# Performance work log

Measured on AMD Instinct MI355X. Metric: run time of the kernel, lower is better.

## Reference

```python
import jax, jax.numpy as jnp
import numpy as np

D_MODEL = 256
NHEAD = 8
DK = D_MODEL // NHEAD
EDGE_FEAT_DIM = 7
N_NODES = 2048
N_EDGES = 65536
LN_EPS = 1e-5


def _ln(x, g, b):
    mu = jnp.mean(x, axis=-1, keepdims=True)
    var = jnp.mean(jnp.square(x - mu), axis=-1, keepdims=True)
    return (x - mu) * jax.lax.rsqrt(var + LN_EPS) * g + b


def setup_inputs() -> dict:
    key = jax.random.key(0)
    ks = jax.random.split(key, 16)
    d, h2 = D_MODEL, 2 * D_MODEL
    s = 0.02
    inp = {
        "h": jax.random.normal(ks[0], (N_NODES, d), jnp.float32),
        "edge_attr": jax.random.normal(ks[1], (N_EDGES, EDGE_FEAT_DIM), jnp.float32),
        # weights stored as (in, out): y = x @ W + b (matches torch Linear math)
        "Wq": s * jax.random.normal(ks[2], (d, d), jnp.float32),
        "bq": jnp.zeros((d,), jnp.float32),
        "Wk": s * jax.random.normal(ks[3], (d, d), jnp.float32),
        "bk": jnp.zeros((d,), jnp.float32),
        "Wv": s * jax.random.normal(ks[4], (d, d), jnp.float32),
        "bv": jnp.zeros((d,), jnp.float32),
        "Wo": s * jax.random.normal(ks[5], (d, d), jnp.float32),
        "bo": jnp.zeros((d,), jnp.float32),
        "We": s * jax.random.normal(ks[6], (EDGE_FEAT_DIM, NHEAD), jnp.float32),
        "be": jnp.zeros((NHEAD,), jnp.float32),
        "ln1_g": jnp.ones((d,), jnp.float32),
        "ln1_b": jnp.zeros((d,), jnp.float32),
        "fln_g": jnp.ones((d,), jnp.float32),
        "fln_b": jnp.zeros((d,), jnp.float32),
        "W1": s * jax.random.normal(ks[7], (d, h2), jnp.float32),
        "b1": jnp.zeros((h2,), jnp.float32),
        "W2": s * jax.random.normal(ks[8], (h2, d), jnp.float32),
        "b2": jnp.zeros((d,), jnp.float32),
        "edge_index": jax.random.randint(ks[9], (2, N_EDGES), 0, N_NODES, jnp.int64 if jax.config.jax_enable_x64 else jnp.int32),
    }
    return inp


def reference(h, edge_attr, Wq, bq, Wk, bk, Wv, bv, Wo, bo, We, be,
              ln1_g, ln1_b, fln_g, fln_b, W1, b1, W2, b2, edge_index):
    N = h.shape[0]
    res = h
    # edge bias scattered into dense (N, N, H) tensor
    eb = edge_attr @ We + be                                  # (E, H)
    attn_bias = jnp.zeros((N, N, NHEAD), h.dtype).at[edge_index[0], edge_index[1]].set(eb)
    Q = (h @ Wq + bq).reshape(N, NHEAD, DK)
    K = (h @ Wk + bk).reshape(N, NHEAD, DK)
    V = (h @ Wv + bv).reshape(N, NHEAD, DK)
    scores = jnp.einsum('nhd,mhd->nmh', Q, K) / jnp.sqrt(jnp.float32(DK)) + attn_bias
    attn = jax.nn.softmax(scores, axis=1)                     # softmax over keys m
    out = jnp.einsum('nmh,mhd->nhd', attn, V).reshape(N, D_MODEL)
    out = out @ Wo + bo
    h1 = _ln(res + out, ln1_g, ln1_b)
    ffn = jax.nn.gelu(_ln(h1, fln_g, fln_b) @ W1 + b1, approximate=False) @ W2 + b2
    return h1 + ffn
```

## Files before the change

kernel.cpp:

```cpp
#include <hip/hip_runtime.h>
#include <math.h>

#define NN 2048
#define NE 65536
#define DM 256
#define NH 8
#define DKH 32
#define CAP 128
#define TM2 128
#define SPLIT 4

typedef __attribute__((ext_vector_type(8))) short bf16x8;
typedef __attribute__((ext_vector_type(4))) float f32x4;

__device__ __forceinline__ unsigned short f2b(float f) {
    unsigned u = __float_as_uint(f);
    unsigned r = (u + 0x7FFFu + ((u >> 16) & 1u)) >> 16;
    return (unsigned short)r;
}
__device__ __forceinline__ float b2f(unsigned short s) {
    return __uint_as_float(((unsigned)s) << 16);
}

__global__ __launch_bounds__(256) void edge_eb_kernel(
    const float* __restrict__ ea, const float* __restrict__ We,
    const float* __restrict__ be, float* __restrict__ eb)
{
    int e = blockIdx.x * 256 + threadIdx.x;
    float acc[NH];
#pragma unroll
    for (int h = 0; h < NH; ++h) acc[h] = be[h];
#pragma unroll
    for (int f = 0; f < 7; ++f) {
        float x = ea[e * 7 + f];
#pragma unroll
        for (int h = 0; h < NH; ++h) acc[h] = fmaf(x, We[f * NH + h], acc[h]);
    }
#pragma unroll
    for (int h = 0; h < NH; ++h) eb[e * NH + h] = acc[h];
}

__global__ __launch_bounds__(256) void scatter_kernel(
    const int* __restrict__ ei, int* __restrict__ cnt, int* __restrict__ lst)
{
    int e = blockIdx.x * 256 + threadIdx.x;
    int s = ei[e];
    int p = atomicAdd(&cnt[s], 1);
    if (p < CAP) lst[s * CAP + p] = e;
}

__global__ __launch_bounds__(128) void rowprep_kernel(
    const int* __restrict__ ei, const int* __restrict__ cnt,
    const int* __restrict__ lst, int* __restrict__ sortedDest,
    int* __restrict__ sortedE, int* __restrict__ rowOff)
{
    __shared__ int ds[CAP], es[CAP];
    __shared__ int bc[16], off[17];
    int n = blockIdx.x, t = threadIdx.x;
    int c = cnt[n]; if (c > CAP) c = CAP;
    if (t < 16) bc[t] = 0;
    int e = -1, d = -1;
    if (t < c) { e = lst[n * CAP + t]; d = ei[NE + e]; }
    ds[t] = d; es[t] = e;
    __syncthreads();
    bool win = (t < c);
    if (win) {
        for (int j = 0; j < c; ++j)
            if (ds[j] == d && es[j] > e) { win = false; break; }
    }
    int bkt = (d >= 0) ? (d >> 7) : 0;
    int pos = -1;
    if (win) pos = atomicAdd(&bc[bkt], 1);
    __syncthreads();
    if (t == 0) {
        int s = 0;
        for (int i = 0; i < 16; ++i) { off[i] = s; s += bc[i]; }
        off[16] = s;
    }
    __syncthreads();
    if (win) {
        int p = off[bkt] + pos;
        sortedDest[n * CAP + p] = d;
        sortedE[n * CAP + p] = e;
    }
    if (t < 17) rowOff[n * 17 + t] = off[t];
}

__global__ __launch_bounds__(256) void conv_h_kernel(
    const float* __restrict__ x, unsigned short* __restrict__ y)
{
    int i = blockIdx.x * 256 + threadIdx.x;
    y[i] = f2b(x[i]);
}

__global__ __launch_bounds__(256) void convT_kernel(
    const float* __restrict__ in, unsigned short* __restrict__ out, int K, int N)
{
    int i = blockIdx.x * 256 + threadIdx.x;
    int n = i / K, k = i - n * K;
    out[i] = f2b(in[(size_t)k * N + n]);
}

__global__ __launch_bounds__(256) void convT_qkv_kernel(
    const float* __restrict__ Wq, const float* __restrict__ Wk,
    const float* __restrict__ Wv, unsigned short* __restrict__ out)
{
    int i = blockIdx.x * 256 + threadIdx.x;
    int n = i >> 8, k = i & 255;
    const float* W = (n < 256) ? Wq : (n < 512) ? Wk : Wv;
    out[i] = f2b(W[k * 256 + (n & 255)]);
}

template <int EPI>
__global__ __launch_bounds__(128) void gemm_bf16(
    const unsigned short* __restrict__ A, const unsigned short* __restrict__ Bt,
    const float* __restrict__ bias0, const float* __restrict__ bias1,
    const float* __restrict__ bias2, const float* __restrict__ resid,
    void* __restrict__ out0, void* __restrict__ out1, void* __restrict__ out2,
    int M, int N, int K)
{
    __shared__ unsigned short As[32][40];
    __shared__ unsigned short Bs[64][40];
    int tid = threadIdx.x;
    int wv = tid >> 6, l = tid & 63, l15 = l & 15, quad = l >> 4;
    int m0 = blockIdx.y * 32, n0 = blockIdx.x * 64;

    f32x4 acc[4];
#pragma unroll
    for (int i = 0; i < 4; ++i) acc[i] = (f32x4){0.f, 0.f, 0.f, 0.f};

    int ra = tid >> 2, ka = (tid & 3) * 8;
    int rb = tid >> 1, kb = (tid & 1) * 16;

    for (int k0 = 0; k0 < K; k0 += 32) {
        *(uint4*)&As[ra][ka] = *(const uint4*)(A + (size_t)(m0 + ra) * K + k0 + ka);
        *(uint4*)&Bs[rb][kb]     = *(const uint4*)(Bt + (size_t)(n0 + rb) * K + k0 + kb);
        *(uint4*)&Bs[rb][kb + 8] = *(const uint4*)(Bt + (size_t)(n0 + rb) * K + k0 + kb + 8);
        __syncthreads();
        bf16x8 a = *(const bf16x8*)&As[wv * 16 + l15][quad * 8];
#pragma unroll
        for (int nt = 0; nt < 4; ++nt) {
            bf16x8 b = *(const bf16x8*)&Bs[nt * 16 + l15][quad * 8];
            acc[nt] = __builtin_amdgcn_mfma_f32_16x16x32_bf16(a, b, acc[nt], 0, 0, 0);
        }
        __syncthreads();
    }

#pragma unroll
    for (int nt = 0; nt < 4; ++nt) {
#pragma unroll
        for (int r = 0; r < 4; ++r) {
            int row = m0 + wv * 16 + quad * 4 + r;
            int col = n0 + nt * 16 + l15;
            float v = acc[nt][r];
            if (EPI == 0) {
                v += bias0[col];
                if (resid) v += resid[(size_t)row * N + col];
                ((float*)out0)[(size_t)row * N + col] = v;
            } else if (EPI == 1) {
                v += bias0[col];
                v = 0.5f * v * (1.0f + erff(v * 0.70710678118654752f));
                ((unsigned short*)out0)[(size_t)row * N + col] = f2b(v);
            } else {
                if (col < 256) {
                    v = (v + bias0[col]) * 0.17677669529663689f;
                    ((unsigned short*)out0)[(size_t)row * 256 + col] = f2b(v);
                } else if (col < 512) {
                    v += bias1[col - 256];
                    ((unsigned short*)out1)[(size_t)row * 256 + col - 256] = f2b(v);
                } else {
                    v += bias2[col - 512];
                    ((unsigned short*)out2)[(size_t)row * 256 + col - 512] = f2b(v);
                }
            }
        }
    }
}

__global__ __launch_bounds__(256) void vtrans_kernel(
    const unsigned short* __restrict__ Vb, unsigned short* __restrict__ Vt)
{
    __shared__ unsigned short tile[64][40];
    int h = blockIdx.y, n0 = blockIdx.x * 64, t = threadIdx.x;
    int r = t >> 2, c8 = (t & 3) * 8;
    *(uint4*)&tile[r][c8] = *(const uint4*)(Vb + (size_t)(n0 + r) * DM + h * 32 + c8);
    __syncthreads();
    int d = t >> 3, nc = (t & 7) * 8;
    unsigned short o[8];
#pragma unroll
    for (int j = 0; j < 8; ++j) o[j] = tile[nc + j][d];
    *(uint4*)(Vt + ((size_t)h * 32 + d) * NN + n0 + nc) = *(uint4*)o;
}

__global__ __launch_bounds__(128) void attn_mfma(
    const unsigned short* __restrict__ Qb, const unsigned short* __restrict__ Kb,
    const unsigned short* __restrict__ Vt, const float* __restrict__ eb,
    const int* __restrict__ sortedDest, const int* __restrict__ sortedE,
    const int* __restrict__ rowOff,
    float* __restrict__ accD, float* __restrict__ lD)
{
    __shared__ unsigned short Ks[TM2][40];
    __shared__ unsigned short Vs[32][TM2 + 8];
    __shared__ unsigned short Ps[2][16][TM2 + 16];
    __shared__ float ldelta[2][16];
    int h = blockIdx.y, tid = threadIdx.x;
    int wv = tid >> 6, l = tid & 63, l15 = l & 15, quad = l >> 4;
    int n0 = blockIdx.x * 32 + wv * 16;
    int mz = blockIdx.z;

    if (l < 16) ldelta[wv][l] = 0.f;

    bf16x8 aq = *(const bf16x8*)(Qb + (size_t)(n0 + l15) * DM + h * 32 + quad * 8);

    f32x4 oacc[2];
    oacc[0] = (f32x4){0.f, 0.f, 0.f, 0.f};
    oacc[1] = (f32x4){0.f, 0.f, 0.f, 0.f};
    float lacc[4] = {0.f, 0.f, 0.f, 0.f};
    const unsigned short* Vth = Vt + (size_t)h * 32 * NN;

    int r16 = l >> 2, sub = l & 3;
    int frow = n0 + r16;

    for (int t = 0; t < NN / (TM2 * SPLIT); ++t) {
        int m0 = (mz * (NN / SPLIT)) + t * TM2;
        int ti = m0 >> 7;
        {
            const unsigned short* ks = Kb + (size_t)(m0 + tid) * DM + h * 32;
            *(uint4*)&Ks[tid][0]  = *(const uint4*)(ks);
            *(uint4*)&Ks[tid][8]  = *(const uint4*)(ks + 8);
            *(uint4*)&Ks[tid][16] = *(const uint4*)(ks + 16);
            *(uint4*)&Ks[tid][24] = *(const uint4*)(ks + 24);
            int d = tid >> 2, mc = (tid & 3) * 32;
            const unsigned short* vs = Vth + (size_t)d * NN + m0 + mc;
            *(uint4*)&Vs[d][mc]      = *(const uint4*)(vs);
            *(uint4*)&Vs[d][mc + 8]  = *(const uint4*)(vs + 8);
            *(uint4*)&Vs[d][mc + 16] = *(const uint4*)(vs + 16);
            *(uint4*)&Vs[d][mc + 24] = *(const uint4*)(vs + 24);
        }
        __syncthreads();
#pragma unroll
        for (int mt = 0; mt < TM2 / 16; ++mt) {
            bf16x8 bk = *(const bf16x8*)&Ks[mt * 16 + l15][quad * 8];
            f32x4 s = __builtin_amdgcn_mfma_f32_16x16x32_bf16(
                aq, bk, (f32x4){0.f, 0.f, 0.f, 0.f}, 0, 0, 0);
#pragma unroll
            for (int r = 0; r < 4; ++r) {
                float p = __expf(s[r]);
                lacc[r] += p;
                Ps[wv][quad * 4 + r][mt * 16 + l15] = f2b(p);
            }
        }
        __syncthreads();
        {
            int o0 = rowOff[frow * 17 + ti];
            int o1 = rowOff[frow * 17 + ti + 1];
            for (int idx = o0 + sub; idx < o1; idx += 4) {
                int d = sortedDest[frow * CAP + idx] - m0;
                int e = sortedE[frow * CAP + idx];
                float expb = __expf(eb[e * NH + h]);
                float pold = b2f(Ps[wv][r16][d]);
                Ps[wv][r16][d] = f2b(pold * expb);
                atomicAdd(&ldelta[wv][r16], pold * (expb - 1.0f));
            }
        }
        __syncthreads();
#pragma unroll
        for (int kc = 0; kc < TM2 / 32; ++kc) {
            bf16x8 ap = *(const bf16x8*)&Ps[wv][l15][kc * 32 + quad * 8];
#pragma unroll
            for (int nt = 0; nt < 2; ++nt) {
                bf16x8 bv = *(const bf16x8*)&Vs[nt * 16 + l15][kc * 32 + quad * 8];
                oacc[nt] = __builtin_amdgcn_mfma_f32_16x16x32_bf16(ap, bv, oacc[nt], 0, 0, 0);
            }
        }
        __syncthreads();
    }

#pragma unroll
    for (int off = 1; off < 16; off <<= 1) {
#pragma unroll
        for (int r = 0; r < 4; ++r) lacc[r] += __shfl_xor(lacc[r], off);
    }
    float* lDp = lD + (size_t)mz * NN * NH;
    if (l15 == 0) {
#pragma unroll
        for (int r = 0; r < 4; ++r)
            lDp[(size_t)(n0 + quad * 4 + r) * NH + h] = lacc[r] + ldelta[wv][quad * 4 + r];
    }
    float* aDp = accD + (size_t)mz * NN * DM;
#pragma unroll
    for (int nt = 0; nt < 2; ++nt)
#pragma unroll
        for (int r = 0; r < 4; ++r)
            aDp[(size_t)(n0 + quad * 4 + r) * DM + h * 32 + nt * 16 + l15] = oacc[nt][r];
}

__global__ __launch_bounds__(256) void norm_kernel(
    const float* __restrict__ accD, const float* __restrict__ lD,
    unsigned short* __restrict__ AOb)
{
    int i = blockIdx.x * 256 + threadIdx.x;
    int n = i >> 8, cdim = i & 255, h = cdim >> 5;
    float o = 0.f, lsum = 0.f;
#pragma unroll
    for (int s = 0; s < SPLIT; ++s) {
        o += accD[(size_t)s * NN * DM + i];
        lsum += lD[(size_t)s * NN * NH + (size_t)n * NH + h];
    }
    AOb[i] = f2b(o / lsum);
}

__global__ __launch_bounds__(256) void ln2_kernel(
    const float* __restrict__ T, const float* __restrict__ g1, const float* __restrict__ b1,
    const float* __restrict__ g2, const float* __restrict__ b2,
    float* __restrict__ H1, unsigned short* __restrict__ X2b)
{
    __shared__ float red[4];
    int n = blockIdx.x, t = threadIdx.x;
    float x = T[(size_t)n * DM + t];

    float s = x;
#pragma unroll
    for (int off = 32; off; off >>= 1) s += __shfl_xor(s, off);
    if ((t & 63) == 0) red[t >> 6] = s;
    __syncthreads();
    float mu = (red[0] + red[1] + red[2] + red[3]) * (1.0f / 256.0f);
    __syncthreads();

    float d = x - mu;
    float v = d * d;
#pragma unroll
    for (int off = 32; off; off >>= 1) v += __shfl_xor(v, off);
    if ((t & 63) == 0) red[t >> 6] = v;
    __syncthreads();
    float var = (red[0] + red[1] + red[2] + red[3]) * (1.0f / 256.0f);
    float y = d * rsqrtf(var + 1e-5f) * g1[t] + b1[t];
    H1[(size_t)n * DM + t] = y;
    __syncthreads();

    float s2 = y;
#pragma unroll
    for (int off = 32; off; off >>= 1) s2 += __shfl_xor(s2, off);
    if ((t & 63) == 0) red[t >> 6] = s2;
    __syncthreads();
    float mu2 = (red[0] + red[1] + red[2] + red[3]) * (1.0f / 256.0f);
    __syncthreads();

    float d2 = y - mu2;
    float v2 = d2 * d2;
#pragma unroll
    for (int off = 32; off; off >>= 1) v2 += __shfl_xor(v2, off);
    if ((t & 63) == 0) red[t >> 6] = v2;
    __syncthreads();
    float var2 = (red[0] + red[1] + red[2] + red[3]) * (1.0f / 256.0f);
    X2b[(size_t)n * DM + t] = f2b(d2 * rsqrtf(var2 + 1e-5f) * g2[t] + b2[t]);
}

extern "C" void kernel_launch(void* const* d_in, const int* in_sizes, int n_in,
                              void* d_out, int out_size, void* d_ws, size_t ws_size,
                              hipStream_t stream)
{
    const float* h    = (const float*)d_in[0];
    const float* ea   = (const float*)d_in[1];
    const float* Wq   = (const float*)d_in[2];
    const float* bq   = (const float*)d_in[3];
    const float* Wk   = (const float*)d_in[4];
    const float* bk   = (const float*)d_in[5];
    const float* Wv   = (const float*)d_in[6];
    const float* bv   = (const float*)d_in[7];
    const float* Wo   = (const float*)d_in[8];
    const float* bo   = (const float*)d_in[9];
    const float* We   = (const float*)d_in[10];
    const float* be   = (const float*)d_in[11];
    const float* ln1g = (const float*)d_in[12];
    const float* ln1b = (const float*)d_in[13];
    const float* flng = (const float*)d_in[14];
    const float* flnb = (const float*)d_in[15];
    const float* W1   = (const float*)d_in[16];
    const float* b1   = (const float*)d_in[17];
    const float* W2   = (const float*)d_in[18];
    const float* b2   = (const float*)d_in[19];
    const int*   ei   = (const int*)d_in[20];
    float* out = (float*)d_out;

    char* p = (char*)d_ws;
    float* eb   = (float*)p;           p += (size_t)NE * NH * 4;
    int*   cnt  = (int*)p;             p += (size_t)NN * 4;
    int*   lst  = (int*)p;             p += (size_t)NN * CAP * 4;
    int*   sD   = (int*)p;             p += (size_t)NN * CAP * 4;
    int*   sE   = (int*)p;             p += (size_t)NN * CAP * 4;
    int*   rOff = (int*)p;             p += (size_t)NN * 17 * 4;
    unsigned short* hb    = (unsigned short*)p; p += (size_t)NN * DM * 2;
    unsigned short* Wqkvt = (unsigned short*)p; p += (size_t)768 * 256 * 2;
    unsigned short* Wot   = (unsigned short*)p; p += (size_t)256 * 256 * 2;
    unsigned short* W1t   = (unsigned short*)p; p += (size_t)512 * 256 * 2;
    unsigned short* W2t   = (unsigned short*)p; p += (size_t)256 * 512 * 2;
    unsigned short* Qb    = (unsigned short*)p; p += (size_t)NN * DM * 2;
    unsigned short* Kb    = (unsigned short*)p; p += (size_t)NN * DM * 2;
    unsigned short* Vb    = (unsigned short*)p; p += (size_t)NN * DM * 2;
    unsigned short* Vt    = (unsigned short*)p; p += (size_t)NN * DM * 2;
    float* accD = (float*)p;           p += (size_t)SPLIT * NN * DM * 4;
    float* lD   = (float*)p;           p += (size_t)SPLIT * NN * NH * 4;
    unsigned short* AOb   = (unsigned short*)p; p += (size_t)NN * DM * 2;
    float* T    = (float*)p;           p += (size_t)NN * DM * 4;
    float* H1   = (float*)p;           p += (size_t)NN * DM * 4;
    unsigned short* X2b   = (unsigned short*)p; p += (size_t)NN * DM * 2;
    unsigned short* F1b   = (unsigned short*)p; p += (size_t)NN * 512 * 2;

    hipMemsetAsync(cnt, 0, (size_t)NN * 4, stream);
    edge_eb_kernel<<<NE / 256, 256, 0, stream>>>(ea, We, be, eb);
    scatter_kernel<<<NE / 256, 256, 0, stream>>>(ei, cnt, lst);
    rowprep_kernel<<<NN, 128, 0, stream>>>(ei, cnt, lst, sD, sE, rOff);

    conv_h_kernel<<<NN * DM / 256, 256, 0, stream>>>(h, hb);
    convT_qkv_kernel<<<768 * 256 / 256, 256, 0, stream>>>(Wq, Wk, Wv, Wqkvt);
    convT_kernel<<<256 * 256 / 256, 256, 0, stream>>>(Wo, Wot, 256, 256);
    convT_kernel<<<512 * 256 / 256, 256, 0, stream>>>(W1, W1t, 256, 512);
    convT_kernel<<<512 * 256 / 256, 256, 0, stream>>>(W2, W2t, 512, 256);

    gemm_bf16<2><<<dim3(768 / 64, NN / 32), 128, 0, stream>>>(
        hb, Wqkvt, bq, bk, bv, nullptr, Qb, Kb, Vb, NN, 768, 256);
    vtrans_kernel<<<dim3(NN / 64, NH), 256, 0, stream>>>(Vb, Vt);

    attn_mfma<<<dim3(NN / 32, NH, SPLIT), 128, 0, stream>>>(
        Qb, Kb, Vt, eb, sD, sE, rOff, accD, lD);
    norm_kernel<<<NN * DM / 256, 256, 0, stream>>>(accD, lD, AOb);

    gemm_bf16<0><<<dim3(256 / 64, NN / 32), 128, 0, stream>>>(
        AOb, Wot, bo, nullptr, nullptr, h, T, nullptr, nullptr, NN, 256, 256);
    ln2_kernel<<<NN, 256, 0, stream>>>(T, ln1g, ln1b, flng, flnb, H1, X2b);

    gemm_bf16<1><<<dim3(512 / 64, NN / 32), 128, 0, stream>>>(
        X2b, W1t, b1, nullptr, nullptr, nullptr, F1b, nullptr, nullptr, NN, 512, 256);
    gemm_bf16<0><<<dim3(256 / 64, NN / 32), 128, 0, stream>>>(
        F1b, W2t, b2, nullptr, nullptr, H1, out, nullptr, nullptr, NN, 256, 512);
}
```

Measured before the change: 204.1 us.

## Fuse prep kernels and enlarge GEMM and attention blocks to four waves

Merges edge-bias computation with edge scatter, and folds the input and weight bf16 conversion and transpose kernels into a single launch. The bf16 GEMM gets a template row-tile size, and the QKV and W1 GEMMs use 64-row tiles with 256 threads. The attention kernel now processes 64 query rows per block with four waves, sharing each K/V tile load across more rows. The aim is less launch overhead and fewer redundant K/V and B loads, at the cost of fewer blocks and possibly lower occupancy.

```diff
diff --git a/kernel.cpp b/kernel.cpp
--- a/kernel.cpp
+++ b/kernel.cpp
@@ -22,9 +22,10 @@
     return __uint_as_float(((unsigned)s) << 16);
 }
 
-__global__ __launch_bounds__(256) void edge_eb_kernel(
+__global__ __launch_bounds__(256) void edge_prep_kernel(
     const float* __restrict__ ea, const float* __restrict__ We,
-    const float* __restrict__ be, float* __restrict__ eb)
+    const float* __restrict__ be, const int* __restrict__ ei,
+    float* __restrict__ eb, int* __restrict__ cnt, int* __restrict__ lst)
 {
     int e = blockIdx.x * 256 + threadIdx.x;
     float acc[NH];
@@ -38,12 +39,6 @@
     }
 #pragma unroll
     for (int h = 0; h < NH; ++h) eb[e * NH + h] = acc[h];
-}
-
-__global__ __launch_bounds__(256) void scatter_kernel(
-    const int* __restrict__ ei, int* __restrict__ cnt, int* __restrict__ lst)
-{
-    int e = blockIdx.x * 256 + threadIdx.x;
     int s = ei[e];
     int p = atomicAdd(&cnt[s], 1);
     if (p < CAP) lst[s * CAP + p] = e;
@@ -86,56 +81,67 @@
     if (t < 17) rowOff[n * 17 + t] = off[t];
 }
 
-__global__ __launch_bounds__(256) void conv_h_kernel(
-    const float* __restrict__ x, unsigned short* __restrict__ y)
+__global__ __launch_bounds__(256) void prep_kernel(
+    const float* __restrict__ h, const float* __restrict__ Wq,
+    const float* __restrict__ Wk, const float* __restrict__ Wv,
+    const float* __restrict__ Wo, const float* __restrict__ W1,
+    const float* __restrict__ W2,
+    unsigned short* __restrict__ hb, unsigned short* __restrict__ Wqkvt,
+    unsigned short* __restrict__ Wot, unsigned short* __restrict__ W1t,
+    unsigned short* __restrict__ W2t)
 {
     int i = blockIdx.x * 256 + threadIdx.x;
-    y[i] = f2b(x[i]);
-}
-
-__global__ __launch_bounds__(256) void convT_kernel(
-    const float* __restrict__ in, unsigned short* __restrict__ out, int K, int N)
-{
-    int i = blockIdx.x * 256 + threadIdx.x;
-    int n = i / K, k = i - n * K;
-    out[i] = f2b(in[(size_t)k * N + n]);
-}
-
-__global__ __launch_bounds__(256) void convT_qkv_kernel(
-    const float* __restrict__ Wq, const float* __restrict__ Wk,
-    const float* __restrict__ Wv, unsigned short* __restrict__ out)
-{
-    int i = blockIdx.x * 256 + threadIdx.x;
-    int n = i >> 8, k = i & 255;
-    const float* W = (n < 256) ? Wq : (n < 512) ? Wk : Wv;
-    out[i] = f2b(W[k * 256 + (n & 255)]);
-}
-
-template <int EPI>
-__global__ __launch_bounds__(128) void gemm_bf16(
+    if (i < 524288) {
+        hb[i] = f2b(h[i]);
+    } else if (i < 720896) {
+        int j = i - 524288;
+        int n = j >> 8, k = j & 255;
+        const float* W = (n < 256) ? Wq : (n < 512) ? Wk : Wv;
+        Wqkvt[j] = f2b(W[k * 256 + (n & 255)]);
+    } else if (i < 786432) {
+        int j = i - 720896;
+        int n = j >> 8, k = j & 255;
+        Wot[j] = f2b(Wo[k * 256 + n]);
+    } else if (i < 917504) {
+        int j = i - 786432;
+        int n = j >> 8, k = j & 255;
+        W1t[j] = f2b(W1[(size_t)k * 512 + n]);
+    } else {
+        int j = i - 917504;
+        int n = j >> 9, k = j & 511;
+        W2t[j] = f2b(W2[(size_t)k * 256 + n]);
+    }
+}
+
+template <int EPI, int MT>
+__global__ __launch_bounds__(MT * 4) void gemm_bf16(
     const unsigned short* __restrict__ A, const unsigned short* __restrict__ Bt,
     const float* __restrict__ bias0, const float* __restrict__ bias1,
     const float* __restrict__ bias2, const float* __restrict__ resid,
     void* __restrict__ out0, void* __restrict__ out1, void* __restrict__ out2,
     int M, int N, int K)
 {
-    __shared__ unsigned short As[32][40];
+    __shared__ unsigned short As[MT][40];
     __shared__ unsigned short Bs[64][40];
     int tid = threadIdx.x;
     int wv = tid >> 6, l = tid & 63, l15 = l & 15, quad = l >> 4;
-    int m0 = blockIdx.y * 32, n0 = blockIdx.x * 64;
+    int m0 = blockIdx.y * MT, n0 = blockIdx.x * 64;
 
     f32x4 acc[4];
 #pragma unroll
     for (int i = 0; i < 4; ++i) acc[i] = (f32x4){0.f, 0.f, 0.f, 0.f};
 
     int ra = tid >> 2, ka = (tid & 3) * 8;
-    int rb = tid >> 1, kb = (tid & 1) * 16;
 
     for (int k0 = 0; k0 < K; k0 += 32) {
         *(uint4*)&As[ra][ka] = *(const uint4*)(A + (size_t)(m0 + ra) * K + k0 + ka);
-        *(uint4*)&Bs[rb][kb]     = *(const uint4*)(Bt + (size_t)(n0 + rb) * K + k0 + kb);
-        *(uint4*)&Bs[rb][kb + 8] = *(const uint4*)(Bt + (size_t)(n0 + rb) * K + k0 + kb + 8);
+        if (MT == 64) {
+            *(uint4*)&Bs[ra][ka] = *(const uint4*)(Bt + (size_t)(n0 + ra) * K + k0 + ka);
+        } else {
+            int rb = tid >> 1, kb = (tid & 1) * 16;
+            *(uint4*)&Bs[rb][kb]     = *(const uint4*)(Bt + (size_t)(n0 + rb) * K + k0 + kb);
+            *(uint4*)&Bs[rb][kb + 8] = *(const uint4*)(Bt + (size_t)(n0 + rb) * K + k0 + kb + 8);
+        }
         __syncthreads();
         bf16x8 a = *(const bf16x8*)&As[wv * 16 + l15][quad * 8];
 #pragma unroll
@@ -192,7 +198,7 @@
     *(uint4*)(Vt + ((size_t)h * 32 + d) * NN + n0 + nc) = *(uint4*)o;
 }
 
-__global__ __launch_bounds__(128) void attn_mfma(
+__global__ __launch_bounds__(256) void attn_mfma(
     const unsigned short* __restrict__ Qb, const unsigned short* __restrict__ Kb,
     const unsigned short* __restrict__ Vt, const float* __restrict__ eb,
     const int* __restrict__ sortedDest, const int* __restrict__ sortedE,
@@ -201,11 +207,11 @@
 {
     __shared__ unsigned short Ks[TM2][40];
     __shared__ unsigned short Vs[32][TM2 + 8];
-    __shared__ unsigned short Ps[2][16][TM2 + 16];
-    __shared__ float ldelta[2][16];
+    __shared__ unsigned short Ps[4][16][TM2 + 16];
+    __shared__ float ldelta[4][16];
     int h = blockIdx.y, tid = threadIdx.x;
     int wv = tid >> 6, l = tid & 63, l15 = l & 15, quad = l >> 4;
-    int n0 = blockIdx.x * 32 + wv * 16;
+    int n0 = blockIdx.x * 64 + wv * 16;
     int mz = blockIdx.z;
 
     if (l < 16) ldelta[wv][l] = 0.f;
@@ -225,17 +231,14 @@
         int m0 = (mz * (NN / SPLIT)) + t * TM2;
         int ti = m0 >> 7;
         {
-            const unsigned short* ks = Kb + (size_t)(m0 + tid) * DM + h * 32;
-            *(uint4*)&Ks[tid][0]  = *(const uint4*)(ks);
-            *(uint4*)&Ks[tid][8]  = *(const uint4*)(ks + 8);
-            *(uint4*)&Ks[tid][16] = *(const uint4*)(ks + 16);
-            *(uint4*)&Ks[tid][24] = *(const uint4*)(ks + 24);
-            int d = tid >> 2, mc = (tid & 3) * 32;
+            int r = tid >> 1, kc = (tid & 1) * 16;
+            const unsigned short* ks = Kb + (size_t)(m0 + r) * DM + h * 32 + kc;
+            *(uint4*)&Ks[r][kc]     = *(const uint4*)(ks);
+            *(uint4*)&Ks[r][kc + 8] = *(const uint4*)(ks + 8);
+            int d = tid >> 3, mc = (tid & 7) * 16;
             const unsigned short* vs = Vth + (size_t)d * NN + m0 + mc;
-            *(uint4*)&Vs[d][mc]      = *(const uint4*)(vs);
-            *(uint4*)&Vs[d][mc + 8]  = *(const uint4*)(vs + 8);
-            *(uint4*)&Vs[d][mc + 16] = *(const uint4*)(vs + 16);
-            *(uint4*)&Vs[d][mc + 24] = *(const uint4*)(vs + 24);
+            *(uint4*)&Vs[d][mc]     = *(const uint4*)(vs);
+            *(uint4*)&Vs[d][mc + 8] = *(const uint4*)(vs + 8);
         }
         __syncthreads();
 #pragma unroll
@@ -408,30 +411,26 @@
     unsigned short* F1b   = (unsigned short*)p; p += (size_t)NN * 512 * 2;
 
     hipMemsetAsync(cnt, 0, (size_t)NN * 4, stream);
-    edge_eb_kernel<<<NE / 256, 256, 0, stream>>>(ea, We, be, eb);
-    scatter_kernel<<<NE / 256, 256, 0, stream>>>(ei, cnt, lst);
+    edge_prep_kernel<<<NE / 256, 256, 0, stream>>>(ea, We, be, ei, eb, cnt, lst);
     rowprep_kernel<<<NN, 128, 0, stream>>>(ei, cnt, lst, sD, sE, rOff);
 
-    conv_h_kernel<<<NN * DM / 256, 256, 0, stream>>>(h, hb);
-    convT_qkv_kernel<<<768 * 256 / 256, 256, 0, stream>>>(Wq, Wk, Wv, Wqkvt);
-    convT_kernel<<<256 * 256 / 256, 256, 0, stream>>>(Wo, Wot, 256, 256);
-    convT_kernel<<<512 * 256 / 256, 256, 0, stream>>>(W1, W1t, 256, 512);
-    convT_kernel<<<512 * 256 / 256, 256, 0, stream>>>(W2, W2t, 512, 256);
-
-    gemm_bf16<2><<<dim3(768 / 64, NN / 32), 128, 0, stream>>>(
+    prep_kernel<<<1048576 / 256, 256, 0, stream>>>(
+        h, Wq, Wk, Wv, Wo, W1, W2, hb, Wqkvt, Wot, W1t, W2t);
+
+    gemm_bf16<2, 64><<<dim3(768 / 64, NN / 64), 256, 0, stream>>>(
         hb, Wqkvt, bq, bk, bv, nullptr, Qb, Kb, Vb, NN, 768, 256);
     vtrans_kernel<<<dim3(NN / 64, NH), 256, 0, stream>>>(Vb, Vt);
 
-    attn_mfma<<<dim3(NN / 32, NH, SPLIT), 128, 0, stream>>>(
+    attn_mfma<<<dim3(NN / 64, NH, SPLIT), 256, 0, stream>>>(
         Qb, Kb, Vt, eb, sD, sE, rOff, accD, lD);
     norm_kernel<<<NN * DM / 256, 256, 0, stream>>>(accD, lD, AOb);
 
-    gemm_bf16<0><<<dim3(256 / 64, NN / 32), 128, 0, stream>>>(
+    gemm_bf16<0, 32><<<dim3(256 / 64, NN / 32), 128, 0, stream>>>(
         AOb, Wot, bo, nullptr, nullptr, h, T, nullptr, nullptr, NN, 256, 256);
     ln2_kernel<<<NN, 256, 0, stream>>>(T, ln1g, ln1b, flng, flnb, H1, X2b);
 
-    gemm_bf16<1><<<dim3(512 / 64, NN / 32), 128, 0, stream>>>(
+    gemm_bf16<1, 64><<<dim3(512 / 64, NN / 64), 256, 0, stream>>>(
         X2b, W1t, b1, nullptr, nullptr, nullptr, F1b, nullptr, nullptr, NN, 512, 256);
-    gemm_bf16<0><<<dim3(256 / 64, NN / 32), 128, 0, stream>>>(
+    gemm_bf16<0, 32><<<dim3(256 / 64, NN / 32), 128, 0, stream>>>(
         F1b, W2t, b2, nullptr, nullptr, H1, out, nullptr, nullptr, NN, 256, 512);
 }
```

Result: faster. 189.0 us (-7.4%).
